# Kernel optimization log

Measured on AMD Instinct MI355X. Metric: run time of the kernel, lower is better.

The kernel has to match this reference:

```python
import jax, jax.numpy as jnp
import numpy as np

SEQ_LEN = 128      # timesteps, each with its OWN Dense (flax compact creates Dense_t per loop iter)
N_FEAT = 512
HIDDEN = 1024
N_ACTORS = 2


def setup_inputs() -> dict:
    key = jax.random.key(0)
    k_x, k_h, k_W, k_b, k_Wo, k_bo = jax.random.split(key, 6)
    x = jax.random.normal(k_x, (1, SEQ_LEN, N_FEAT), dtype=jnp.float32)
    h = jax.random.normal(k_h, (HIDDEN,), dtype=jnp.float32)
    # One distinct Dense per timestep: kernel (N_FEAT+HIDDEN, HIDDEN), bias (HIDDEN,)
    scale = 1.0 / np.sqrt(N_FEAT + HIDDEN)
    Ws = jax.random.normal(k_W, (SEQ_LEN, N_FEAT + HIDDEN, HIDDEN), dtype=jnp.float32) * scale
    bs = jnp.zeros((SEQ_LEN, HIDDEN), dtype=jnp.float32)
    W_out = jax.random.normal(k_Wo, (HIDDEN, N_ACTORS), dtype=jnp.float32) * (1.0 / np.sqrt(HIDDEN))
    b_out = jnp.zeros((N_ACTORS,), dtype=jnp.float32)
    return {"x": x, "h": h, "Ws": Ws, "bs": bs, "W_out": W_out, "b_out": b_out}


def reference(x, h, Ws, bs, W_out, b_out):
    # x: (1, T, F); h: (H,); Ws: (T, F+H, H); bs: (T, H)
    xs = jnp.swapaxes(x, 0, 1)  # (T, 1, F) -> scan over time

    def step(h_carry, inputs):
        xt, W, b = inputs  # xt: (1, F), W: (F+H, H), b: (H,)
        z = jnp.concatenate([xt, h_carry[None, :]], axis=-1)  # (1, F+H)
        h_new = jnp.tanh(z @ W + b).squeeze()                  # (H,)
        return h_new, None

    h_final, _ = jax.lax.scan(step, h, (xs, Ws, bs))
    actors = h_final @ W_out + b_out  # (N_ACTORS,)
    return (actors, h_final)
```

## Files before the change

kernel.cpp:

```cpp
#include <hip/hip_runtime.h>
#include <math.h>

#define TT 128
#define NF 512
#define HH 1024
#define WROWS (NF + HH)
#define SPIN_LIMIT (1 << 22)

__global__ __launch_bounds__(256) void pg_phase1(
    const float* __restrict__ x, const float* __restrict__ Ws,
    const float* __restrict__ bs, float* __restrict__ acc,
    int* __restrict__ cnt, int* __restrict__ ready) {
  const int t = blockIdx.x >> 2;
  const int q = blockIdx.x & 3;
  const int tid = threadIdx.x;
  __shared__ float xs[NF];
  xs[tid] = x[t * NF + tid];
  xs[tid + 256] = x[t * NF + tid + 256];
  if (q == 0 && tid < 32) cnt[t * 32 + tid] = 0;
  if (q == 1 && tid < 32) ready[t * 32 + tid] = 0;
  __syncthreads();
  const int j = q * 256 + tid;
  const float* w = Ws + (size_t)t * WROWS * HH + j;
  float s = bs[t * HH + j];
#pragma unroll 8
  for (int k = 0; k < NF; ++k) s += xs[k] * w[(size_t)k * HH];
  acc[t * HH + j] = s;
}

__global__ __launch_bounds__(256) void pg_phase2(
    const float* __restrict__ h_in, const float* __restrict__ Ws,
    const float* __restrict__ Wout, const float* __restrict__ bout,
    float* __restrict__ acc, float* __restrict__ h_buf,
    int* __restrict__ cnt, int* __restrict__ ready,
    float* __restrict__ out) {
  const int tid = threadIdx.x;
  const int g = blockIdx.x & 31;
  const int r = blockIdx.x >> 5;
  const int c4 = tid & 7;
  const int rw = tid >> 3;
  const int j0 = g * 32 + c4 * 4;

  __shared__ float hs[128];
  __shared__ float pacc[32][33];
  __shared__ int last_flag;

  const size_t WSTEP = (size_t)WROWS * HH;
  const float* Wb = Ws + (size_t)NF * HH + (size_t)(r * 128 + rw) * HH + j0;

  float4 wb0 = *(const float4*)(Wb);
  float4 wb1 = *(const float4*)(Wb + 32 * HH);
  float4 wb2 = *(const float4*)(Wb + 64 * HH);
  float4 wb3 = *(const float4*)(Wb + 96 * HH);

  for (int t = 0; t < TT; ++t) {
    float4 w0 = wb0, w1 = wb1, w2 = wb2, w3 = wb3;
    if (t + 1 < TT) {
      const float* p = Wb + (size_t)(t + 1) * WSTEP;
      wb0 = *(const float4*)(p);
      wb1 = *(const float4*)(p + 32 * HH);
      wb2 = *(const float4*)(p + 64 * HH);
      wb3 = *(const float4*)(p + 96 * HH);
    }
    if (t == 0) {
      if (tid < 128) hs[tid] = h_in[r * 128 + tid];
      __syncthreads();
    } else {
      if (tid < 4) {
        const int* f = &ready[(t - 1) * 32 + r * 4 + tid];
        int guard = 0;
        while (__hip_atomic_load(f, __ATOMIC_ACQUIRE,
                                 __HIP_MEMORY_SCOPE_AGENT) == 0 &&
               ++guard < SPIN_LIMIT)
          __builtin_amdgcn_s_sleep(1);
      }
      __syncthreads();
      if (tid < 128)
        hs[tid] = __hip_atomic_load(
            &h_buf[(size_t)(t - 1) * HH + r * 128 + tid], __ATOMIC_RELAXED,
            __HIP_MEMORY_SCOPE_AGENT);
      __syncthreads();
    }

    const float h0 = hs[rw], h1 = hs[rw + 32], h2 = hs[rw + 64],
                h3 = hs[rw + 96];
    pacc[rw][c4 * 4 + 0] = h0 * w0.x + h1 * w1.x + h2 * w2.x + h3 * w3.x;
    pacc[rw][c4 * 4 + 1] = h0 * w0.y + h1 * w1.y + h2 * w2.y + h3 * w3.y;
    pacc[rw][c4 * 4 + 2] = h0 * w0.z + h1 * w1.z + h2 * w2.z + h3 * w3.z;
    pacc[rw][c4 * 4 + 3] = h0 * w0.w + h1 * w1.w + h2 * w2.w + h3 * w3.w;
    __syncthreads();

    if (tid < 32) {
      float s = 0.f;
#pragma unroll
      for (int rr = 0; rr < 32; ++rr) s += pacc[rr][tid];
      atomicAdd(&acc[(size_t)t * HH + g * 32 + tid], s);
    }
    if (tid == 0) {
      int old = __hip_atomic_fetch_add(&cnt[t * 32 + g], 1, __ATOMIC_ACQ_REL,
                                       __HIP_MEMORY_SCOPE_AGENT);
      last_flag = (old == 7);
    }
    __syncthreads();

    if (last_flag) {
      if (tid < 32) {
        float v = __hip_atomic_load(&acc[(size_t)t * HH + g * 32 + tid],
                                    __ATOMIC_RELAXED, __HIP_MEMORY_SCOPE_AGENT);
        float hv = tanhf(v);
        __hip_atomic_store(&h_buf[(size_t)t * HH + g * 32 + tid], hv,
                           __ATOMIC_RELAXED, __HIP_MEMORY_SCOPE_AGENT);
      }
      __threadfence();
      if (tid == 0)
        __hip_atomic_store(&ready[t * 32 + g], 1, __ATOMIC_RELEASE,
                           __HIP_MEMORY_SCOPE_AGENT);
    }
  }

  if (blockIdx.x == 0) {
    if (tid < 32) {
      const int* f = &ready[(TT - 1) * 32 + tid];
      int guard = 0;
      while (__hip_atomic_load(f, __ATOMIC_ACQUIRE,
                               __HIP_MEMORY_SCOPE_AGENT) == 0 &&
             ++guard < SPIN_LIMIT)
        __builtin_amdgcn_s_sleep(1);
    }
    __syncthreads();
    float a0 = 0.f, a1 = 0.f;
#pragma unroll
    for (int i = 0; i < 4; ++i) {
      int k = tid + 256 * i;
      float v = __hip_atomic_load(&h_buf[(size_t)(TT - 1) * HH + k],
                                  __ATOMIC_RELAXED, __HIP_MEMORY_SCOPE_AGENT);
      out[2 + k] = v;
      a0 += v * Wout[k * 2 + 0];
      a1 += v * Wout[k * 2 + 1];
    }
    float* red = &pacc[0][0];
    red[tid] = a0;
    red[256 + tid] = a1;
    __syncthreads();
    for (int s = 128; s > 0; s >>= 1) {
      if (tid < s) {
        red[tid] += red[tid + s];
        red[256 + tid] += red[256 + tid + s];
      }
      __syncthreads();
    }
    if (tid == 0) {
      out[0] = red[0] + bout[0];
      out[1] = red[256] + bout[1];
    }
  }
}

extern "C" void kernel_launch(void* const* d_in, const int* in_sizes, int n_in,
                              void* d_out, int out_size, void* d_ws,
                              size_t ws_size, hipStream_t stream) {
  const float* x = (const float*)d_in[0];
  const float* h = (const float*)d_in[1];
  const float* Ws = (const float*)d_in[2];
  const float* bs = (const float*)d_in[3];
  const float* Wout = (const float*)d_in[4];
  const float* bout = (const float*)d_in[5];
  float* out = (float*)d_out;

  float* acc = (float*)d_ws;
  float* h_buf = acc + TT * HH;
  int* cnt = (int*)(h_buf + TT * HH);
  int* ready = cnt + TT * 32;

  pg_phase1<<<dim3(TT * 4), dim3(256), 0, stream>>>(x, Ws, bs, acc, cnt,
                                                    ready);
  pg_phase2<<<dim3(256), dim3(256), 0, stream>>>(h, Ws, Wout, bout, acc, h_buf,
                                                 cnt, ready, out);
}
```

Before: 4.252 ms.

## Fuse input projection into persistent recurrent kernel with per-column-block flags

Drops the separate input-projection kernel and computes x·W_x inside the persistent recurrent kernel. Each of 256 blocks now owns 4 output columns and covers all 1536 rows, so there are no cross-block atomicAdd partial sums or counters. Partial sums are reduced with wave shuffles, and each block waits on all 256 per-block ready flags from the previous step. This removes the atomic accumulation and last-block election from the serial critical path. In exchange, every block loads the full previous h vector each step, each thread polls one flag, and the 4-column float4 loads are strided, which may hurt memory coalescing.

New measurement: 3.888 ms. 1.09x faster.

```diff
diff --git a/kernel.cpp b/kernel.cpp
--- a/kernel.cpp
+++ b/kernel.cpp
@@ -5,140 +5,145 @@
 #define NF 512
 #define HH 1024
 #define WROWS (NF + HH)
+#define NB 256
+#define COLS 4
 #define SPIN_LIMIT (1 << 22)
 
-__global__ __launch_bounds__(256) void pg_phase1(
-    const float* __restrict__ x, const float* __restrict__ Ws,
-    const float* __restrict__ bs, float* __restrict__ acc,
-    int* __restrict__ cnt, int* __restrict__ ready) {
-  const int t = blockIdx.x >> 2;
-  const int q = blockIdx.x & 3;
-  const int tid = threadIdx.x;
-  __shared__ float xs[NF];
-  xs[tid] = x[t * NF + tid];
-  xs[tid + 256] = x[t * NF + tid + 256];
-  if (q == 0 && tid < 32) cnt[t * 32 + tid] = 0;
-  if (q == 1 && tid < 32) ready[t * 32 + tid] = 0;
-  __syncthreads();
-  const int j = q * 256 + tid;
-  const float* w = Ws + (size_t)t * WROWS * HH + j;
-  float s = bs[t * HH + j];
-#pragma unroll 8
-  for (int k = 0; k < NF; ++k) s += xs[k] * w[(size_t)k * HH];
-  acc[t * HH + j] = s;
+__device__ __forceinline__ void spin_flag(const int* __restrict__ f) {
+  int guard = 0;
+  while (__hip_atomic_load(f, __ATOMIC_RELAXED, __HIP_MEMORY_SCOPE_AGENT) ==
+         0) {
+    if (++guard >= SPIN_LIMIT) break;
+    if ((guard & 127) == 0)
+      (void)__hip_atomic_load(f, __ATOMIC_ACQUIRE, __HIP_MEMORY_SCOPE_AGENT);
+    __builtin_amdgcn_s_sleep(1);
+  }
+  (void)__hip_atomic_load(f, __ATOMIC_ACQUIRE, __HIP_MEMORY_SCOPE_AGENT);
 }
 
-__global__ __launch_bounds__(256) void pg_phase2(
-    const float* __restrict__ h_in, const float* __restrict__ Ws,
+__device__ __forceinline__ void rnn_step(
+    const int t, float4 (&CUR)[6], float4 (&NXT)[6], const float xc0,
+    const float xc1, const float bc, float& xn0, float& xn1, float& bn,
+    const float* __restrict__ Wb, const float* __restrict__ x,
+    const float* __restrict__ h_in, const float* __restrict__ bs,
+    float* __restrict__ h_buf, int* __restrict__ ready,
+    float* __restrict__ out, float (*pacc)[COLS], const int tid, const int g,
+    const int gcol0, const int w) {
+  const size_t WSTEP = (size_t)WROWS * HH;
+
+  if (t + 1 < TT) {
+    const float* p = Wb + (size_t)(t + 1) * WSTEP;
+#pragma unroll
+    for (int i = 0; i < 6; ++i)
+      NXT[i] = *(const float4*)(p + (size_t)(i * 256) * HH);
+    xn0 = x[(t + 1) * NF + tid];
+    xn1 = x[(t + 1) * NF + 256 + tid];
+    bn = bs[(t + 1) * HH + gcol0 + (tid & 3)];
+  }
+
+  float h0, h1, h2, h3;
+  if (t == 0) {
+    h0 = h_in[tid];
+    h1 = h_in[256 + tid];
+    h2 = h_in[512 + tid];
+    h3 = h_in[768 + tid];
+  } else {
+    spin_flag(&ready[(t - 1) * NB + tid]);
+    __syncthreads();
+    const float* hb = h_buf + (size_t)(t - 1) * HH;
+    h0 = __hip_atomic_load(hb + tid, __ATOMIC_RELAXED,
+                           __HIP_MEMORY_SCOPE_AGENT);
+    h1 = __hip_atomic_load(hb + 256 + tid, __ATOMIC_RELAXED,
+                           __HIP_MEMORY_SCOPE_AGENT);
+    h2 = __hip_atomic_load(hb + 512 + tid, __ATOMIC_RELAXED,
+                           __HIP_MEMORY_SCOPE_AGENT);
+    h3 = __hip_atomic_load(hb + 768 + tid, __ATOMIC_RELAXED,
+                           __HIP_MEMORY_SCOPE_AGENT);
+  }
+
+  float4 s;
+  s.x = xc0 * CUR[0].x + xc1 * CUR[1].x + h0 * CUR[2].x + h1 * CUR[3].x +
+        h2 * CUR[4].x + h3 * CUR[5].x;
+  s.y = xc0 * CUR[0].y + xc1 * CUR[1].y + h0 * CUR[2].y + h1 * CUR[3].y +
+        h2 * CUR[4].y + h3 * CUR[5].y;
+  s.z = xc0 * CUR[0].z + xc1 * CUR[1].z + h0 * CUR[2].z + h1 * CUR[3].z +
+        h2 * CUR[4].z + h3 * CUR[5].z;
+  s.w = xc0 * CUR[0].w + xc1 * CUR[1].w + h0 * CUR[2].w + h1 * CUR[3].w +
+        h2 * CUR[4].w + h3 * CUR[5].w;
+
+#pragma unroll
+  for (int m = 1; m <= 32; m <<= 1) {
+    s.x += __shfl_xor(s.x, m);
+    s.y += __shfl_xor(s.y, m);
+    s.z += __shfl_xor(s.z, m);
+    s.w += __shfl_xor(s.w, m);
+  }
+  if ((tid & 63) == 0) {
+    pacc[w][0] = s.x;
+    pacc[w][1] = s.y;
+    pacc[w][2] = s.z;
+    pacc[w][3] = s.w;
+  }
+  __syncthreads();
+
+  if (tid < COLS) {
+    const float v =
+        pacc[0][tid] + pacc[1][tid] + pacc[2][tid] + pacc[3][tid] + bc;
+    const float hv = tanhf(v);
+    __hip_atomic_store(&h_buf[(size_t)t * HH + gcol0 + tid], hv,
+                       __ATOMIC_RELAXED, __HIP_MEMORY_SCOPE_AGENT);
+    if (t == TT - 1) out[2 + gcol0 + tid] = hv;
+  }
+  if (tid == 0)
+    __hip_atomic_store(&ready[t * NB + g], 1, __ATOMIC_RELEASE,
+                       __HIP_MEMORY_SCOPE_AGENT);
+}
+
+__global__ __launch_bounds__(256, 1) void pg_rnn(
+    const float* __restrict__ x, const float* __restrict__ h_in,
+    const float* __restrict__ Ws, const float* __restrict__ bs,
     const float* __restrict__ Wout, const float* __restrict__ bout,
-    float* __restrict__ acc, float* __restrict__ h_buf,
-    int* __restrict__ cnt, int* __restrict__ ready,
+    float* __restrict__ h_buf, int* __restrict__ ready,
     float* __restrict__ out) {
   const int tid = threadIdx.x;
-  const int g = blockIdx.x & 31;
-  const int r = blockIdx.x >> 5;
-  const int c4 = tid & 7;
-  const int rw = tid >> 3;
-  const int j0 = g * 32 + c4 * 4;
+  const int g = blockIdx.x;
+  const int w = tid >> 6;
+  const int gcol0 = g * COLS;
 
-  __shared__ float hs[128];
-  __shared__ float pacc[32][33];
-  __shared__ int last_flag;
+  __shared__ float pacc[4][COLS];
+  __shared__ float red[512];
 
-  const size_t WSTEP = (size_t)WROWS * HH;
-  const float* Wb = Ws + (size_t)NF * HH + (size_t)(r * 128 + rw) * HH + j0;
+  const float* Wb = Ws + (size_t)tid * HH + gcol0;
 
-  float4 wb0 = *(const float4*)(Wb);
-  float4 wb1 = *(const float4*)(Wb + 32 * HH);
-  float4 wb2 = *(const float4*)(Wb + 64 * HH);
-  float4 wb3 = *(const float4*)(Wb + 96 * HH);
+  float4 A[6], B[6];
+  float xa0, xa1, xb0, xb1, ba, bb;
+#pragma unroll
+  for (int i = 0; i < 6; ++i)
+    A[i] = *(const float4*)(Wb + (size_t)(i * 256) * HH);
+  xa0 = x[tid];
+  xa1 = x[256 + tid];
+  ba = bs[gcol0 + (tid & 3)];
 
-  for (int t = 0; t < TT; ++t) {
-    float4 w0 = wb0, w1 = wb1, w2 = wb2, w3 = wb3;
-    if (t + 1 < TT) {
-      const float* p = Wb + (size_t)(t + 1) * WSTEP;
-      wb0 = *(const float4*)(p);
-      wb1 = *(const float4*)(p + 32 * HH);
-      wb2 = *(const float4*)(p + 64 * HH);
-      wb3 = *(const float4*)(p + 96 * HH);
-    }
-    if (t == 0) {
-      if (tid < 128) hs[tid] = h_in[r * 128 + tid];
-      __syncthreads();
-    } else {
-      if (tid < 4) {
-        const int* f = &ready[(t - 1) * 32 + r * 4 + tid];
-        int guard = 0;
-        while (__hip_atomic_load(f, __ATOMIC_ACQUIRE,
-                                 __HIP_MEMORY_SCOPE_AGENT) == 0 &&
-               ++guard < SPIN_LIMIT)
-          __builtin_amdgcn_s_sleep(1);
-      }
-      __syncthreads();
-      if (tid < 128)
-        hs[tid] = __hip_atomic_load(
-            &h_buf[(size_t)(t - 1) * HH + r * 128 + tid], __ATOMIC_RELAXED,
-            __HIP_MEMORY_SCOPE_AGENT);
-      __syncthreads();
-    }
-
-    const float h0 = hs[rw], h1 = hs[rw + 32], h2 = hs[rw + 64],
-                h3 = hs[rw + 96];
-    pacc[rw][c4 * 4 + 0] = h0 * w0.x + h1 * w1.x + h2 * w2.x + h3 * w3.x;
-    pacc[rw][c4 * 4 + 1] = h0 * w0.y + h1 * w1.y + h2 * w2.y + h3 * w3.y;
-    pacc[rw][c4 * 4 + 2] = h0 * w0.z + h1 * w1.z + h2 * w2.z + h3 * w3.z;
-    pacc[rw][c4 * 4 + 3] = h0 * w0.w + h1 * w1.w + h2 * w2.w + h3 * w3.w;
-    __syncthreads();
-
-    if (tid < 32) {
-      float s = 0.f;
-#pragma unroll
-      for (int rr = 0; rr < 32; ++rr) s += pacc[rr][tid];
-      atomicAdd(&acc[(size_t)t * HH + g * 32 + tid], s);
-    }
-    if (tid == 0) {
-      int old = __hip_atomic_fetch_add(&cnt[t * 32 + g], 1, __ATOMIC_ACQ_REL,
-                                       __HIP_MEMORY_SCOPE_AGENT);
-      last_flag = (old == 7);
-    }
-    __syncthreads();
-
-    if (last_flag) {
-      if (tid < 32) {
-        float v = __hip_atomic_load(&acc[(size_t)t * HH + g * 32 + tid],
-                                    __ATOMIC_RELAXED, __HIP_MEMORY_SCOPE_AGENT);
-        float hv = tanhf(v);
-        __hip_atomic_store(&h_buf[(size_t)t * HH + g * 32 + tid], hv,
-                           __ATOMIC_RELAXED, __HIP_MEMORY_SCOPE_AGENT);
-      }
-      __threadfence();
-      if (tid == 0)
-        __hip_atomic_store(&ready[t * 32 + g], 1, __ATOMIC_RELEASE,
-                           __HIP_MEMORY_SCOPE_AGENT);
-    }
+  for (int t = 0; t < TT; t += 2) {
+    rnn_step(t, A, B, xa0, xa1, ba, xb0, xb1, bb, Wb, x, h_in, bs, h_buf,
+             ready, out, pacc, tid, g, gcol0, w);
+    rnn_step(t + 1, B, A, xb0, xb1, bb, xa0, xa1, ba, Wb, x, h_in, bs, h_buf,
+             ready, out, pacc, tid, g, gcol0, w);
   }
 
-  if (blockIdx.x == 0) {
-    if (tid < 32) {
-      const int* f = &ready[(TT - 1) * 32 + tid];
-      int guard = 0;
-      while (__hip_atomic_load(f, __ATOMIC_ACQUIRE,
-                               __HIP_MEMORY_SCOPE_AGENT) == 0 &&
-             ++guard < SPIN_LIMIT)
-        __builtin_amdgcn_s_sleep(1);
-    }
+  if (g == 0) {
+    spin_flag(&ready[(TT - 1) * NB + tid]);
     __syncthreads();
     float a0 = 0.f, a1 = 0.f;
 #pragma unroll
     for (int i = 0; i < 4; ++i) {
-      int k = tid + 256 * i;
-      float v = __hip_atomic_load(&h_buf[(size_t)(TT - 1) * HH + k],
-                                  __ATOMIC_RELAXED, __HIP_MEMORY_SCOPE_AGENT);
-      out[2 + k] = v;
+      const int k = tid + 256 * i;
+      const float v =
+          __hip_atomic_load(&h_buf[(size_t)(TT - 1) * HH + k],
+                            __ATOMIC_RELAXED, __HIP_MEMORY_SCOPE_AGENT);
       a0 += v * Wout[k * 2 + 0];
       a1 += v * Wout[k * 2 + 1];
     }
-    float* red = &pacc[0][0];
     red[tid] = a0;
     red[256 + tid] = a1;
     __syncthreads();
@@ -167,13 +172,10 @@
   const float* bout = (const float*)d_in[5];
   float* out = (float*)d_out;
 
-  float* acc = (float*)d_ws;
-  float* h_buf = acc + TT * HH;
-  int* cnt = (int*)(h_buf + TT * HH);
-  int* ready = cnt + TT * 32;
+  float* h_buf = (float*)d_ws;
+  int* ready = (int*)(h_buf + TT * HH);
 
-  pg_phase1<<<dim3(TT * 4), dim3(256), 0, stream>>>(x, Ws, bs, acc, cnt,
-                                                    ready);
-  pg_phase2<<<dim3(256), dim3(256), 0, stream>>>(h, Ws, Wout, bout, acc, h_buf,
-                                                 cnt, ready, out);
+  hipMemsetAsync(ready, 0, TT * NB * sizeof(int), stream);
+  pg_rnn<<<dim3(NB), dim3(256), 0, stream>>>(x, h, Ws, bs, Wout, bout, h_buf,
+                                             ready, out);
 }
```
